# Optimization experiments

Hardware: AMD Instinct MI355X
Metric: run time of the kernel (lower is better)

Reference implementation:

```python
import jax, jax.numpy as jnp
import numpy as np

B, T, D = 2, 2048, 1024
NH, NKV, HD, RD = 16, 4, 64, 32


def apply_rope(x, cos, sin):
    # x: [B, H, T, hd]; cos/sin: [T, 1, 1, RD//2]
    r = cos.shape[-1] * 2
    x1 = x[..., : r // 2]
    x2 = x[..., r // 2 : r]
    x_pass = x[..., r:]
    c = cos.reshape(1, 1, cos.shape[0], -1)  # [1,1,T,RD//2]
    s = sin.reshape(1, 1, sin.shape[0], -1)
    return jnp.concatenate([x1 * c - x2 * s, x1 * s + x2 * c, x_pass], axis=-1)


def setup_inputs() -> dict:
    key = jax.random.key(0)
    ks = jax.random.split(key, 8)
    # realistic partial-RoPE angle tables
    inv_freq = 1.0 / (10000.0 ** (np.arange(0, RD, 2, dtype=np.float32) / RD))
    ang = np.arange(T, dtype=np.float32)[:, None] * inv_freq[None, :]  # [T, RD//2]
    cos = jnp.asarray(np.cos(ang)).reshape(T, 1, 1, RD // 2)
    sin = jnp.asarray(np.sin(ang)).reshape(T, 1, 1, RD // 2)
    return {
        "x": jax.random.normal(ks[0], (B, T, D), dtype=jnp.float32),
        "cos": cos,
        "sin": sin,
        "v0": jax.random.normal(ks[1], (B, NH, T, HD), dtype=jnp.float32),
        "Wqkv": jax.random.normal(ks[2], ((NH + 2 * NKV) * HD, D), dtype=jnp.float32) * (D ** -0.5),
        "Wproj": jax.random.normal(ks[3], (D, D), dtype=jnp.float32) * (D ** -0.5),
        "vrl_alpha": jnp.full((NH,), 0.1, dtype=jnp.float32),
        "qk_scale": 0.5 + jax.random.uniform(ks[4], (NH,), dtype=jnp.float32),
    }


def reference(x, cos, sin, v0, Wqkv, Wproj, vrl_alpha, qk_scale):
    nH, nKV, hd = NH, NKV, HD
    qkv = jnp.einsum("btd,ed->bte", x, Wqkv)  # [B,T,(nH+2nKV)*hd]
    q = qkv[..., : nH * hd].reshape(B, T, nH, hd).transpose(0, 2, 1, 3)
    k = qkv[..., nH * hd : (nH + nKV) * hd].reshape(B, T, nKV, hd).transpose(0, 2, 1, 3)
    v = qkv[..., (nH + nKV) * hd :].reshape(B, T, nKV, hd).transpose(0, 2, 1, 3)
    q = apply_rope(q, cos, sin)
    k = apply_rope(k, cos, sin)
    reps = nH // nKV
    k_exp = jnp.repeat(k, reps, axis=1)  # [B,nH,T,hd]
    v_exp = jnp.repeat(v, reps, axis=1)
    # VRL blend (layer_idx > 0)
    alpha = jax.nn.sigmoid(vrl_alpha)[None, :, None, None]
    v_exp = (1.0 - alpha) * v_exp + alpha * v0
    # per-head learned qk scale, split as sqrt on q and k
    sfac = jnp.sqrt(qk_scale[None, :, None, None] * (hd ** -0.5))
    q_s = q * sfac
    k_s = k_exp * sfac
    # causal SDPA (default scale 1/sqrt(hd))
    scores = jnp.einsum("bhqd,bhkd->bhqk", q_s, k_s) * (hd ** -0.5)
    causal = jnp.tril(jnp.ones((T, T), dtype=bool))
    scores = jnp.where(causal[None, None], scores, jnp.float32(-1e30))
    attn = jax.nn.softmax(scores, axis=-1)
    y = jnp.einsum("bhqk,bhkd->bhqd", attn, v_exp)
    y = y.transpose(0, 2, 1, 3).reshape(B, T, D)
    out = jnp.einsum("btd,ed->bte", y, Wproj)
    return out, v0
```

## Files before the change

kernel.cpp:

```cpp
#include <hip/hip_runtime.h>
#include <hip/hip_bf16.h>

#define B_   2
#define T_   2048
#define D_   1024
#define NH_  16
#define NKV_ 4
#define HD_  64
#define E_   1536
#define LOG2E 1.4426950408889634f

typedef __attribute__((ext_vector_type(8))) __bf16 bf16x8;
typedef __attribute__((ext_vector_type(4))) __bf16 bf16x4;
typedef __attribute__((ext_vector_type(4))) float f32x4;

static __device__ __forceinline__ void gld_lds16(const unsigned short* g, unsigned short* l) {
  __builtin_amdgcn_global_load_lds(
      (const __attribute__((address_space(1))) unsigned int*)(unsigned long long)(const void*)g,
      (__attribute__((address_space(3))) unsigned int*)(unsigned int)(unsigned long long)(void*)l,
      16, 0, 0);
}

static __device__ __forceinline__ float fexp2(float x) {
  float r; asm("v_exp_f32 %0, %1" : "=v"(r) : "v"(x)); return r;
}
static __device__ __forceinline__ float fmax3(float a, float b, float c) {
  float r; asm("v_max3_f32 %0, %1, %2, %3" : "=v"(r) : "v"(a), "v"(b), "v"(c)); return r;
}
static __device__ __forceinline__ float frcp(float x) {
  float r; asm("v_rcp_f32 %0, %1" : "=v"(r) : "v"(x)); return r;
}

#define CVT8(dst, f0, f1) {                                                    \
  dst[0] = (__bf16)f0.x; dst[1] = (__bf16)f0.y;                               \
  dst[2] = (__bf16)f0.z; dst[3] = (__bf16)f0.w;                               \
  dst[4] = (__bf16)f1.x; dst[5] = (__bf16)f1.y;                               \
  dst[6] = (__bf16)f1.z; dst[7] = (__bf16)f1.w; }

__global__ void k_convert_w(const float* __restrict__ wq, const float* __restrict__ wp,
                            unsigned short* __restrict__ wqb, unsigned short* __restrict__ wpb) {
  int i = blockIdx.x * blockDim.x + threadIdx.x;
  const float* src; unsigned short* dst; int j;
  if (i < 196608) { src = wq; dst = wqb; j = i; }
  else            { src = wp; dst = wpb; j = i - 196608; }
  int n = j >> 7, c8 = (j & 127) * 8;
  const float4* p = (const float4*)(src + (size_t)n * 1024 + c8);
  float4 a = p[0], b = p[1];
  bf16x8 o; CVT8(o, a, b);
  *(bf16x8*)(dst + (size_t)n * 1024 + (c8 ^ ((n & 7) * 8))) = o;
}

__global__ __launch_bounds__(256) void k_gemm_qkv(
    const float* __restrict__ X,
    const unsigned short* __restrict__ W,
    const float* __restrict__ cosT, const float* __restrict__ sinT,
    const float* __restrict__ v0,
    const float* __restrict__ vrl, const float* __restrict__ qks,
    unsigned short* __restrict__ qb, unsigned short* __restrict__ kb,
    unsigned short* __restrict__ vb) {
  __shared__ __align__(16) unsigned short As[2][128 * 64];
  __shared__ __align__(16) unsigned short Ws[2][64 * 64];
  int tid = threadIdx.x;
  int w = tid >> 6, l = tid & 63, lo = l & 15, hi = l >> 4;
  int f = blockIdx.y * 24 + blockIdx.x;
  int f2 = (f & 7) * 96 + (f >> 3);
  int bn = f2 % 24, bm = f2 / 24;

  const float* Xb = X + (size_t)bm * 128 * 1024;
  const unsigned short* Wb = W + (size_t)bn * 64 * 1024;

  f32x4 acc[2][4];
#pragma unroll
  for (int mi = 0; mi < 2; ++mi)
#pragma unroll
    for (int ni = 0; ni < 4; ++ni) acc[mi][ni] = (f32x4){0.f, 0.f, 0.f, 0.f};

  int ar = tid >> 2, ac = (tid & 3) * 16;
  int asw = (ar & 7) * 8;
  int acs = ac ^ asw;
  int rsw = (lo & 7) * 8;
  float4 fa[2][4];

#define LOADA(kt) {                                                            \
  int k0 = (kt) * 64;                                                         \
  _Pragma("unroll") for (int ii = 0; ii < 2; ++ii)                            \
  _Pragma("unroll") for (int j = 0; j < 4; ++j)                               \
    fa[ii][j] = *(const float4*)(Xb + (size_t)(ar + ii * 64) * 1024 + k0 + ac + j * 4); }

#define WRITEA(buf) {                                                          \
  _Pragma("unroll") for (int ii = 0; ii < 2; ++ii) {                          \
    bf16x8 o0, o1;                                                            \
    CVT8(o0, fa[ii][0], fa[ii][1]); CVT8(o1, fa[ii][2], fa[ii][3]);           \
    *(bf16x8*)&As[buf][(ar + ii * 64) * 64 + acs] = o0;                       \
    *(bf16x8*)&As[buf][(ar + ii * 64) * 64 + (acs ^ 8)] = o1; } }

#define STAGEW(kt, buf) {                                                      \
  int k0 = (kt) * 64;                                                         \
  _Pragma("unroll") for (int ii = 0; ii < 2; ++ii) {                          \
    int sb = ii * 256 + w * 64;                                               \
    gld_lds16(Wb + (size_t)((sb + l) >> 3) * 1024 + k0 + ((sb + l) & 7) * 8,  \
              &Ws[buf][sb * 8]); } }

  LOADA(0); STAGEW(0, 0); WRITEA(0);
  __syncthreads();

  for (int kt = 0; kt < 16; ++kt) {
    int cur = kt & 1;
    bool pf = (kt + 1) < 16;
    if (pf) { LOADA(kt + 1); STAGEW(kt + 1, cur ^ 1); }
    __builtin_amdgcn_s_setprio(1);
#pragma unroll
    for (int kk = 0; kk < 2; ++kk) {
      int c0 = (kk * 32 + hi * 8) ^ rsw;
      bf16x8 af0 = *(const bf16x8*)&As[cur][(w * 32 + lo) * 64 + c0];
      bf16x8 af1 = *(const bf16x8*)&As[cur][(w * 32 + 16 + lo) * 64 + c0];
#pragma unroll
      for (int ni = 0; ni < 4; ++ni) {
        bf16x8 wf = *(const bf16x8*)&Ws[cur][(ni * 16 + lo) * 64 + c0];
        acc[0][ni] = __builtin_amdgcn_mfma_f32_16x16x32_bf16(af0, wf, acc[0][ni], 0, 0, 0);
        acc[1][ni] = __builtin_amdgcn_mfma_f32_16x16x32_bf16(af1, wf, acc[1][ni], 0, 0, 0);
      }
    }
    __builtin_amdgcn_s_setprio(0);
    if (pf) WRITEA(cur ^ 1);
    __syncthreads();
  }
#undef LOADA
#undef WRITEA
#undef STAGEW

  if (bn < 20) {
    int isq = (bn < 16);
    int h = isq ? bn : bn - 16;
    float sc = isq ? (qks[h] * (LOG2E / 64.0f)) : 1.0f;
    unsigned short* base = isq ? qb : kb;
    int nheads = isq ? NH_ : NKV_;
#pragma unroll
    for (int mi = 0; mi < 2; ++mi) {
#pragma unroll
      for (int r = 0; r < 4; ++r) {
        int row = bm * 128 + w * 32 + mi * 16 + hi * 4 + r;
        int b = row >> 11, t = row & 2047;
        float c = cosT[t * 16 + lo], s = sinT[t * 16 + lo];
        float a0 = acc[mi][0][r], a1 = acc[mi][1][r];
        __bf16* dp = (__bf16*)(base + ((size_t)(b * nheads + h) * T_ + t) * 64);
        int ts = isq ? 0 : (8 * (t & 7));
        dp[lo ^ ts]        = (__bf16)((a0 * c - a1 * s) * sc);
        dp[(16 + lo) ^ ts] = (__bf16)((a0 * s + a1 * c) * sc);
        dp[(32 + lo) ^ ts] = (__bf16)(acc[mi][2][r] * sc);
        dp[(48 + lo) ^ ts] = (__bf16)(acc[mi][3][r] * sc);
      }
    }
  } else {
    int hv = bn - 20;
    float av[4];
#pragma unroll
    for (int j = 0; j < 4; ++j) av[j] = 1.0f / (1.0f + __expf(-vrl[hv * 4 + j]));
#pragma unroll
    for (int mi = 0; mi < 2; ++mi) {
      int t0g = bm * 128 + w * 32 + mi * 16 + hi * 4;
      int b = t0g >> 11, t0 = t0g & 2047;
#pragma unroll
      for (int ni = 0; ni < 4; ++ni) {
        int d = ni * 16 + lo;
#pragma unroll
        for (int j = 0; j < 4; ++j) {
          float a = av[j], na = 1.0f - a;
          const float* v0p = v0 + ((size_t)(b * NH_ + hv * 4 + j) * T_ + t0) * 64 + d;
          bf16x4 vv;
#pragma unroll
          for (int r = 0; r < 4; ++r)
            vv[r] = (__bf16)(na * acc[mi][ni][r] + a * v0p[(size_t)r * 64]);
          *(bf16x4*)((unsigned short*)vb + ((size_t)(b * NH_ + hv * 4 + j) * 64 + d) * T_ +
                     (t0 ^ (8 * (lo & 7)))) = vv;
        }
      }
    }
  }
}

__global__ __launch_bounds__(256) void k_gemm_proj(
    const unsigned short* __restrict__ A,
    const unsigned short* __restrict__ W,
    const float* __restrict__ v0,
    float* __restrict__ C, float* __restrict__ out2) {
  __shared__ __align__(16) unsigned short As[2][128 * 64];
  __shared__ __align__(16) unsigned short Ws[2][64 * 64];
  int tid = threadIdx.x;

  if (blockIdx.y >= 32) {
    int idx = ((blockIdx.y - 32) * 16 + blockIdx.x) * 256 + tid;
    const float4* src = (const float4*)v0;
    float4* dst = (float4*)out2;
#pragma unroll
    for (int i = 0; i < 32; ++i) dst[idx + i * 32768] = src[idx + i * 32768];
    return;
  }

  int w = tid >> 6, l = tid & 63, lo = l & 15, hi = l >> 4;
  int f = blockIdx.y * 16 + blockIdx.x;
  int f2 = (f & 7) * 64 + (f >> 3);
  int bn = f2 & 15, bm = f2 >> 4;
  int rsw = (lo & 7) * 8;

  const unsigned short* Ab = A + (size_t)bm * 128 * 1024;
  const unsigned short* Wb = W + (size_t)bn * 64 * 1024;

  f32x4 acc[2][4];
#pragma unroll
  for (int mi = 0; mi < 2; ++mi)
#pragma unroll
    for (int ni = 0; ni < 4; ++ni) acc[mi][ni] = (f32x4){0.f, 0.f, 0.f, 0.f};

#define STAGE(kt, buf) {                                                       \
  int k0 = (kt) * 64;                                                         \
  _Pragma("unroll") for (int ii = 0; ii < 4; ++ii) {                          \
    int sb = ii * 256 + w * 64;                                               \
    gld_lds16(Ab + (size_t)((sb + l) >> 3) * 1024 + k0 + ((sb + l) & 7) * 8,  \
              &As[buf][sb * 8]); }                                            \
  _Pragma("unroll") for (int ii = 0; ii < 2; ++ii) {                          \
    int sb = ii * 256 + w * 64;                                               \
    gld_lds16(Wb + (size_t)((sb + l) >> 3) * 1024 + k0 + ((sb + l) & 7) * 8,  \
              &Ws[buf][sb * 8]); } }

  STAGE(0, 0);
  __syncthreads();
  for (int kt = 0; kt < 16; ++kt) {
    int cur = kt & 1;
    bool pf = (kt + 1) < 16;
    if (pf) STAGE(kt + 1, cur ^ 1);
    __builtin_amdgcn_s_setprio(1);
#pragma unroll
    for (int kk = 0; kk < 2; ++kk) {
      int c0 = (kk * 32 + hi * 8) ^ rsw;
      bf16x8 af0 = *(const bf16x8*)&As[cur][(w * 32 + lo) * 64 + c0];
      bf16x8 af1 = *(const bf16x8*)&As[cur][(w * 32 + 16 + lo) * 64 + c0];
#pragma unroll
      for (int ni = 0; ni < 4; ++ni) {
        bf16x8 wf = *(const bf16x8*)&Ws[cur][(ni * 16 + lo) * 64 + c0];
        acc[0][ni] = __builtin_amdgcn_mfma_f32_16x16x32_bf16(af0, wf, acc[0][ni], 0, 0, 0);
        acc[1][ni] = __builtin_amdgcn_mfma_f32_16x16x32_bf16(af1, wf, acc[1][ni], 0, 0, 0);
      }
    }
    __builtin_amdgcn_s_setprio(0);
    __syncthreads();
  }
#undef STAGE

#pragma unroll
  for (int mi = 0; mi < 2; ++mi) {
#pragma unroll
    for (int r = 0; r < 4; ++r) {
      int row = bm * 128 + w * 32 + mi * 16 + hi * 4 + r;
      float* cp = C + (size_t)row * D_ + bn * 64 + lo;
#pragma unroll
      for (int ni = 0; ni < 4; ++ni) cp[ni * 16] = acc[mi][ni][r];
    }
  }
}

static __device__ __forceinline__ void stage_kv8(const unsigned short* Kb, const unsigned short* Vb,
                                                 int kv0, int w, int l,
                                                 unsigned short* KsB, unsigned short* VsB) {
  gld_lds16(Kb + (size_t)kv0 * 64 + w * 512 + l * 8, KsB + w * 512);
  gld_lds16(Vb + (size_t)(w * 8 + (l >> 3)) * T_ + kv0 + (l & 7) * 8, VsB + w * 512);
}

__device__ __forceinline__ void softmax_state(f32x4 (&s)[4], float& m, float& lsum,
                                              f32x4 (&y)[4], unsigned short* PsW,
                                              int lo, int hi, int swz) {
  float a0 = fmax3(s[0][0], s[0][1], s[0][2]);
  float a1 = fmax3(s[0][3], s[1][0], s[1][1]);
  float a2 = fmax3(s[1][2], s[1][3], s[2][0]);
  float a3 = fmax3(s[2][1], s[2][2], s[2][3]);
  float a4 = fmax3(s[3][0], s[3][1], s[3][2]);
  float pm = fmaxf(fmax3(a0, a1, a2), fmax3(a3, a4, s[3][3]));
  if (!__all(pm <= m + 8.0f)) {
    pm = fmaxf(pm, __shfl_xor(pm, 16));
    pm = fmaxf(pm, __shfl_xor(pm, 32));
    float mnew = fmaxf(m, pm);
    float sc = fexp2(m - mnew);
    lsum *= sc;
#pragma unroll
    for (int r = 0; r < 4; ++r) {
      float scr = __shfl(sc, hi * 4 + r);
#pragma unroll
      for (int nf = 0; nf < 4; ++nf) y[nf][r] *= scr;
    }
    m = mnew;
  }
  float rs = 0.f;
#pragma unroll
  for (int nt = 0; nt < 4; ++nt) {
    float p0 = fexp2(s[nt][0] - m);
    float p1 = fexp2(s[nt][1] - m);
    float p2 = fexp2(s[nt][2] - m);
    float p3 = fexp2(s[nt][3] - m);
    rs += (p0 + p1) + (p2 + p3);
    bf16x4 pk;
    pk[0] = (__bf16)p0; pk[1] = (__bf16)p1; pk[2] = (__bf16)p2; pk[3] = (__bf16)p3;
    *(bf16x4*)(PsW + lo * 64 + ((nt * 16 + hi * 4) ^ swz)) = pk;
  }
  lsum += rs;
}

__global__ __launch_bounds__(512, 4) void k_attn(const unsigned short* __restrict__ Q,
                                                 const unsigned short* __restrict__ Kp,
                                                 const unsigned short* __restrict__ Vtp,
                                                 unsigned short* __restrict__ Y) {
  int p = blockIdx.x, h = blockIdx.y, b = blockIdx.z;
  if (b == 1) p = 15 - p;
  int tid = threadIdx.x;
  int w = tid >> 6, l = tid & 63, lo = l & 15, hi = l >> 4;
  int kh = h >> 2;
  int qtA = p, qtB = 31 - p;
  int ntB = qtB + 1;
  int st = w >> 2, wq = w & 3;
  int qt = st ? qtA : qtB;
  int q0 = qt * 64 + wq * 16;
  int swz = 8 * (lo & 7);

  __shared__ __align__(16) unsigned short Ks[2][4096];
  __shared__ __align__(16) unsigned short Vs[2][4096];
  __shared__ __align__(16) unsigned short Ps[8192];
  unsigned short* PsW = &Ps[w * 1024];

  const unsigned short* Qb = Q + ((size_t)(b * NH_ + h) * T_) * 64;
  const unsigned short* Kb = Kp + ((size_t)(b * NKV_ + kh) * T_) * 64;
  const unsigned short* Vb = Vtp + ((size_t)(b * NH_ + h) * 64) * T_;

  bf16x8 q_0 = *(const bf16x8*)(Qb + (size_t)(q0 + lo) * 64 + hi * 8);
  bf16x8 q_1 = *(const bf16x8*)(Qb + (size_t)(q0 + lo) * 64 + 32 + hi * 8);

  f32x4 y[4];
#pragma unroll
  for (int nf = 0; nf < 4; ++nf) y[nf] = (f32x4){0.f, 0.f, 0.f, 0.f};
  float m = -INFINITY, lsum = 0.f;

  stage_kv8(Kb, Vb, 0, w, l, Ks[0], Vs[0]);
  __syncthreads();
  int cur = 0;

  for (int kt = 0; kt < ntB; ++kt) {
    bool pf = (kt + 1) < ntB;
    if (pf) stage_kv8(Kb, Vb, (kt + 1) * 64, w, l, Ks[cur ^ 1], Vs[cur ^ 1]);

    if (kt <= qt) {
      int kv0 = kt * 64;
      const unsigned short* KsC = Ks[cur];
      const unsigned short* VsC = Vs[cur];

      f32x4 s[4];
      __builtin_amdgcn_s_setprio(1);
#pragma unroll
      for (int nt = 0; nt < 4; ++nt) {
        int rrow = (nt * 16 + lo) * 64;
        int c0 = (hi * 8) ^ swz;
        bf16x8 kf0 = *(const bf16x8*)&KsC[rrow + c0];
        bf16x8 kf1 = *(const bf16x8*)&KsC[rrow + (c0 ^ 32)];
        f32x4 a = (f32x4){0.f, 0.f, 0.f, 0.f};
        a = __builtin_amdgcn_mfma_f32_16x16x32_bf16(kf0, q_0, a, 0, 0, 0);
        a = __builtin_amdgcn_mfma_f32_16x16x32_bf16(kf1, q_1, a, 0, 0, 0);
        s[nt] = a;
      }
      __builtin_amdgcn_s_setprio(0);

      if (kt == qt) {
#pragma unroll
        for (int nt = 0; nt < 4; ++nt)
#pragma unroll
          for (int r = 0; r < 4; ++r)
            if (kv0 + nt * 16 + hi * 4 + r > q0 + lo) s[nt][r] = -1e30f;
      }

      softmax_state(s, m, lsum, y, PsW, lo, hi, swz);

      __builtin_amdgcn_s_setprio(1);
#pragma unroll
      for (int kc = 0; kc < 2; ++kc) {
        int pcol = (kc * 32 + hi * 8) ^ swz;
        bf16x8 pa = *(const bf16x8*)&PsW[lo * 64 + pcol];
#pragma unroll
        for (int nf = 0; nf < 4; ++nf) {
          bf16x8 vf = *(const bf16x8*)&VsC[(nf * 16 + lo) * 64 + pcol];
          y[nf] = __builtin_amdgcn_mfma_f32_16x16x32_bf16(pa, vf, y[nf], 0, 0, 0);
        }
      }
      __builtin_amdgcn_s_setprio(0);
    }

    __syncthreads();
    cur ^= 1;
  }

  lsum += __shfl_xor(lsum, 16);
  lsum += __shfl_xor(lsum, 32);
  float inv = frcp(lsum);
#pragma unroll
  for (int r = 0; r < 4; ++r) {
    float iv = __shfl(inv, hi * 4 + r);
    int t = q0 + hi * 4 + r;
    int sw = 8 * (t & 7);
    __bf16* yp = (__bf16*)(Y + ((size_t)(b * T_ + t)) * D_ + h * 64);
#pragma unroll
    for (int nf = 0; nf < 4; ++nf)
      yp[(nf * 16 + lo) ^ sw] = (__bf16)(y[nf][r] * iv);
  }
}

extern "C" void kernel_launch(void* const* d_in, const int* in_sizes, int n_in,
                              void* d_out, int out_size, void* d_ws, size_t ws_size,
                              hipStream_t stream) {
  const float* x     = (const float*)d_in[0];
  const float* cosT  = (const float*)d_in[1];
  const float* sinT  = (const float*)d_in[2];
  const float* v0    = (const float*)d_in[3];
  const float* Wqkv  = (const float*)d_in[4];
  const float* Wproj = (const float*)d_in[5];
  const float* vrl   = (const float*)d_in[6];
  const float* qks   = (const float*)d_in[7];
  float* out = (float*)d_out;

  char* ws = (char*)d_ws;
  unsigned short* wqkvb  = (unsigned short*)ws;
  unsigned short* wprojb = (unsigned short*)(ws + 3145728);
  unsigned short* qb     = (unsigned short*)(ws + 5242880);
  unsigned short* kb     = (unsigned short*)(ws + 13631488);
  unsigned short* vb     = (unsigned short*)(ws + 15728640);
  unsigned short* yb     = (unsigned short*)(ws + 24117248);

  k_convert_w<<<1280, 256, 0, stream>>>(Wqkv, Wproj, wqkvb, wprojb);

  k_gemm_qkv<<<dim3(24, 32), 256, 0, stream>>>(x, wqkvb, cosT, sinT, v0, vrl, qks, qb, kb, vb);

  k_attn<<<dim3(16, NH_, B_), 512, 0, stream>>>(qb, kb, vb, yb);

  k_gemm_proj<<<dim3(16, 40), 256, 0, stream>>>(yb, wprojb, v0, out, out + 4194304);
}
```

Before: 107.5 us.

## Pre-convert activations to bf16 and stage A tile via direct global-to-LDS loads

Extends the conversion kernel so it also turns x into swizzled bf16, and the QKV GEMM now stages the A tile with global_load_lds DMA, matching how W is already loaded. This removes the register round trip and the in-loop fp32-to-bf16 conversion, which were re-done for each of the 24 column blocks. The cost is an extra full pass over x in the convert kernel, plus a bf16 buffer written to and read back from HBM. Workspace offsets are shifted to make room for the new buffer.

```diff
diff --git a/kernel.cpp b/kernel.cpp
--- a/kernel.cpp
+++ b/kernel.cpp
@@ -37,12 +37,15 @@
   dst[4] = (__bf16)f1.x; dst[5] = (__bf16)f1.y;                               \
   dst[6] = (__bf16)f1.z; dst[7] = (__bf16)f1.w; }
 
-__global__ void k_convert_w(const float* __restrict__ wq, const float* __restrict__ wp,
-                            unsigned short* __restrict__ wqb, unsigned short* __restrict__ wpb) {
+__global__ void k_convert_all(const float* __restrict__ x, const float* __restrict__ wq,
+                              const float* __restrict__ wp,
+                              unsigned short* __restrict__ xb, unsigned short* __restrict__ wqb,
+                              unsigned short* __restrict__ wpb) {
   int i = blockIdx.x * blockDim.x + threadIdx.x;
   const float* src; unsigned short* dst; int j;
-  if (i < 196608) { src = wq; dst = wqb; j = i; }
-  else            { src = wp; dst = wpb; j = i - 196608; }
+  if (i < 524288)      { src = x;  dst = xb;  j = i; }
+  else if (i < 720896) { src = wq; dst = wqb; j = i - 524288; }
+  else                 { src = wp; dst = wpb; j = i - 720896; }
   int n = j >> 7, c8 = (j & 127) * 8;
   const float4* p = (const float4*)(src + (size_t)n * 1024 + c8);
   float4 a = p[0], b = p[1];
@@ -51,7 +54,7 @@
 }
 
 __global__ __launch_bounds__(256) void k_gemm_qkv(
-    const float* __restrict__ X,
+    const unsigned short* __restrict__ A,
     const unsigned short* __restrict__ W,
     const float* __restrict__ cosT, const float* __restrict__ sinT,
     const float* __restrict__ v0,
@@ -65,8 +68,9 @@
   int f = blockIdx.y * 24 + blockIdx.x;
   int f2 = (f & 7) * 96 + (f >> 3);
   int bn = f2 % 24, bm = f2 / 24;
-
-  const float* Xb = X + (size_t)bm * 128 * 1024;
+  int rsw = (lo & 7) * 8;
+
+  const unsigned short* Ab = A + (size_t)bm * 128 * 1024;
   const unsigned short* Wb = W + (size_t)bn * 64 * 1024;
 
   f32x4 acc[2][4];
@@ -75,39 +79,24 @@
 #pragma unroll
     for (int ni = 0; ni < 4; ++ni) acc[mi][ni] = (f32x4){0.f, 0.f, 0.f, 0.f};
 
-  int ar = tid >> 2, ac = (tid & 3) * 16;
-  int asw = (ar & 7) * 8;
-  int acs = ac ^ asw;
-  int rsw = (lo & 7) * 8;
-  float4 fa[2][4];
-
-#define LOADA(kt) {                                                            \
+#define STAGE(kt, buf) {                                                       \
   int k0 = (kt) * 64;                                                         \
-  _Pragma("unroll") for (int ii = 0; ii < 2; ++ii)                            \
-  _Pragma("unroll") for (int j = 0; j < 4; ++j)                               \
-    fa[ii][j] = *(const float4*)(Xb + (size_t)(ar + ii * 64) * 1024 + k0 + ac + j * 4); }
-
-#define WRITEA(buf) {                                                          \
-  _Pragma("unroll") for (int ii = 0; ii < 2; ++ii) {                          \
-    bf16x8 o0, o1;                                                            \
-    CVT8(o0, fa[ii][0], fa[ii][1]); CVT8(o1, fa[ii][2], fa[ii][3]);           \
-    *(bf16x8*)&As[buf][(ar + ii * 64) * 64 + acs] = o0;                       \
-    *(bf16x8*)&As[buf][(ar + ii * 64) * 64 + (acs ^ 8)] = o1; } }
-
-#define STAGEW(kt, buf) {                                                      \
-  int k0 = (kt) * 64;                                                         \
+  _Pragma("unroll") for (int ii = 0; ii < 4; ++ii) {                          \
+    int sb = ii * 256 + w * 64;                                               \
+    gld_lds16(Ab + (size_t)((sb + l) >> 3) * 1024 + k0 + ((sb + l) & 7) * 8,  \
+              &As[buf][sb * 8]); }                                            \
   _Pragma("unroll") for (int ii = 0; ii < 2; ++ii) {                          \
     int sb = ii * 256 + w * 64;                                               \
     gld_lds16(Wb + (size_t)((sb + l) >> 3) * 1024 + k0 + ((sb + l) & 7) * 8,  \
               &Ws[buf][sb * 8]); } }
 
-  LOADA(0); STAGEW(0, 0); WRITEA(0);
+  STAGE(0, 0);
   __syncthreads();
 
   for (int kt = 0; kt < 16; ++kt) {
     int cur = kt & 1;
     bool pf = (kt + 1) < 16;
-    if (pf) { LOADA(kt + 1); STAGEW(kt + 1, cur ^ 1); }
+    if (pf) STAGE(kt + 1, cur ^ 1);
     __builtin_amdgcn_s_setprio(1);
 #pragma unroll
     for (int kk = 0; kk < 2; ++kk) {
@@ -122,12 +111,9 @@
       }
     }
     __builtin_amdgcn_s_setprio(0);
-    if (pf) WRITEA(cur ^ 1);
     __syncthreads();
   }
-#undef LOADA
-#undef WRITEA
-#undef STAGEW
+#undef STAGE
 
   if (bn < 20) {
     int isq = (bn < 16);
@@ -422,16 +408,17 @@
   float* out = (float*)d_out;
 
   char* ws = (char*)d_ws;
-  unsigned short* wqkvb  = (unsigned short*)ws;
-  unsigned short* wprojb = (unsigned short*)(ws + 3145728);
-  unsigned short* qb     = (unsigned short*)(ws + 5242880);
-  unsigned short* kb     = (unsigned short*)(ws + 13631488);
-  unsigned short* vb     = (unsigned short*)(ws + 15728640);
-  unsigned short* yb     = (unsigned short*)(ws + 24117248);
-
-  k_convert_w<<<1280, 256, 0, stream>>>(Wqkv, Wproj, wqkvb, wprojb);
-
-  k_gemm_qkv<<<dim3(24, 32), 256, 0, stream>>>(x, wqkvb, cosT, sinT, v0, vrl, qks, qb, kb, vb);
+  unsigned short* xb     = (unsigned short*)ws;
+  unsigned short* wqkvb  = (unsigned short*)(ws + 8388608);
+  unsigned short* wprojb = (unsigned short*)(ws + 11534336);
+  unsigned short* qb     = (unsigned short*)(ws + 13631488);
+  unsigned short* kb     = (unsigned short*)(ws + 22020096);
+  unsigned short* vb     = (unsigned short*)(ws + 24117248);
+  unsigned short* yb     = (unsigned short*)(ws + 32505856);
+
+  k_convert_all<<<3328, 256, 0, stream>>>(x, Wqkv, Wproj, xb, wqkvb, wprojb);
+
+  k_gemm_qkv<<<dim3(24, 32), 256, 0, stream>>>(xb, wqkvb, cosT, sinT, v0, vrl, qks, qb, kb, vb);
 
   k_attn<<<dim3(16, NH_, B_), 512, 0, stream>>>(qb, kb, vb, yb);
 
```

Measured after the change: 96.20 us. 1.12x faster.
